# Kernel tuning notes

Hardware: AMD Instinct MI355X
Metric: run time of the kernel (lower is better)

The kernel has to match this reference:

```python
import jax, jax.numpy as jnp
import numpy as np

NUM_CAPS_OUT = 10
NUM_NODES = 32 * 6 * 6  # 1152
IN_DIM = 8
OUT_DIM = 16
ROUTING_ITERS = 3


def squash(x):
    # scale = |x|^2/(1+|x|^2); out = scale * x/|x|  (no epsilon, faithful to torch)
    sn = jnp.sum(x * x, axis=-1, keepdims=True)
    return sn / (1.0 + sn) * x / jnp.sqrt(sn)


def setup_inputs() -> dict:
    key = jax.random.key(0)
    ks = jax.random.split(key, 6)
    B = 512
    images = jax.random.normal(ks[0], (B, 1, 28, 28), dtype=jnp.float32)
    # ConvLayer: Conv2d(1, 256, k=9, s=1) with bias
    conv1_w = jax.random.normal(ks[1], (256, 1, 9, 9), dtype=jnp.float32) * 0.05
    conv1_b = jnp.zeros((256,), dtype=jnp.float32)
    prim_w = jax.random.normal(ks[2], (8 * 32, 256, 9, 9), dtype=jnp.float32) * 0.01
    prim_b = jnp.zeros((8 * 32,), dtype=jnp.float32)
    # DigitCaps weight: torch.randn(10, 1152, 8, 16)
    W = jax.random.normal(ks[3], (NUM_CAPS_OUT, NUM_NODES, IN_DIM, OUT_DIM), dtype=jnp.float32)
    return {"images": images, "conv1_w": conv1_w, "conv1_b": conv1_b,
            "prim_w": prim_w, "prim_b": prim_b, "W": W}


def reference(images, conv1_w, conv1_b, prim_w, prim_b, W):
    B = images.shape[0]
    dn = ('NCHW', 'OIHW', 'NCHW')
    # ConvLayer: 28x28 -> 20x20, 256 channels, ReLU
    x = jax.lax.conv_general_dilated(images, conv1_w, (1, 1), 'VALID', dimension_numbers=dn)
    x = jax.nn.relu(x + conv1_b[None, :, None, None])  # [B,256,20,20]
    # PrimaryCaps: 8 stacked convs -> [B, 8*32, 6, 6]; each capsule viewed as (32*6*6,)
    u = jax.lax.conv_general_dilated(x, prim_w, (2, 2), 'VALID', dimension_numbers=dn)
    u = u + prim_b[None, :, None, None]
    u = u.reshape(B, 8, NUM_NODES).transpose(0, 2, 1)  # [B,1152,8]
    u = squash(u)
    # DigitCaps: u_hat[c,b,n,o] = sum_i u[b,n,i] * W[c,n,i,o]
    u_hat = jnp.einsum('bni,cnio->cbno', u, W)  # [10,B,1152,16]
    # Dynamic routing (3 iterations). b_ij kept as [...,1]: torch replicates it
    # across the 16 out dims identically, so math is unchanged.
    b_ij = jnp.zeros(u_hat.shape[:-1] + (1,), dtype=u_hat.dtype)
    v_j = None
    for it in range(ROUTING_ITERS):
        c_ij = jax.nn.softmax(b_ij, axis=2)            # softmax over nodes
        s_j = jnp.sum(c_ij * u_hat, axis=2, keepdims=True)  # [10,B,1,16]
        v_j = squash(s_j)
        if it < ROUTING_ITERS - 1:
            a_ij = jnp.sum(u_hat * v_j, axis=-1, keepdims=True)  # [10,B,1152,1]
            b_ij = b_ij + a_ij
    # squeeze -> [10,B,16], transpose(0,1) -> [B,10,16]
    return v_j[:, :, 0, :].transpose(1, 0, 2)
```

## Files before the change

### kernel.cpp

```cpp
#include <hip/hip_runtime.h>
#include <hip/hip_bf16.h>
#include <cstddef>
#include <cstdint>

typedef __attribute__((ext_vector_type(8))) short v8s;
typedef __attribute__((ext_vector_type(16))) float v16f;

#define GLDS(SRC, DST) __builtin_amdgcn_global_load_lds( \
    (const __attribute__((address_space(1))) void*)(SRC), \
    (__attribute__((address_space(3))) void*)(DST), 16, 0, 0)

__device__ __forceinline__ void bf16split(float x, unsigned short& h, unsigned short& l) {
    union { float f; unsigned u; } a; a.f = x;
    unsigned r = a.u + 0x7fff + ((a.u >> 16) & 1);
    h = (unsigned short)(r >> 16);
    union { unsigned u; float f; } hb; hb.u = (unsigned)h << 16;
    union { float f; unsigned u; } b; b.f = x - hb.f;
    unsigned r2 = b.u + 0x7fff + ((b.u >> 16) & 1);
    l = (unsigned short)(r2 >> 16);
}

__global__ __launch_bounds__(256) void prep_kernel(
    const float* __restrict__ cw, const float* __restrict__ pw,
    float* __restrict__ wT1, char* __restrict__ wpk)
{
    int idx = blockIdx.x * 256 + threadIdx.x;
    if (idx < 81 * 256) {
        int k = idx >> 8, oc = idx & 255;
        wT1[idx] = cw[oc * 81 + k];
    }
    int Q = idx & 2047;
    int slab = idx >> 11;
    int D = Q << 4;
    int R = D >> 9;
    int v = (D & 511) ^ ((R & 31) << 4);
    int h = v >> 7, pl = (v >> 6) & 1, icb = v & 63;
    int ch = h * 64 + R;
    int g = slab / 81, k = slab - g * 81;
    int ic0 = g * 32 + (icb >> 1);
    const float* src = pw + ((size_t)ch * 256 + ic0) * 81 + k;
    v8s ov;
#pragma unroll
    for (int j = 0; j < 8; ++j) {
        unsigned short hh, ll; bf16split(src[(size_t)j * 81], hh, ll);
        ov[j] = (short)(pl ? ll : hh);
    }
    *(v8s*)(wpk + (size_t)slab * 32768 + D) = ov;
}

__global__ __launch_bounds__(256) void conv1_kernel(
    const float* __restrict__ img,
    const float* __restrict__ wT1,
    const float* __restrict__ bias,
    char* __restrict__ xc2,
    int b0)
{
    const int bl = blockIdx.x;
    const int oc = threadIdx.x;
    __shared__ __align__(16) float im[784];
    const float* ib = img + (size_t)(b0 + bl) * 784;
    for (int e = oc; e < 784; e += 256) im[e] = ib[e];
    float w[81];
#pragma unroll
    for (int k = 0; k < 81; ++k) w[k] = wT1[k * 256 + oc];
    float bv = bias[oc];
    __syncthreads();
    char* ob = xc2 + (size_t)bl * 409600;
    for (int oy = 0; oy < 20; ++oy) {
        float a[20];
#pragma unroll
        for (int ox = 0; ox < 20; ++ox) a[ox] = bv;
        for (int ky = 0; ky < 9; ++ky) {
            const float* rp = &im[(oy + ky) * 28];
            float r[28];
#pragma unroll
            for (int q = 0; q < 7; ++q) {
                float4 v4 = *(const float4*)(rp + q * 4);
                r[q * 4] = v4.x; r[q * 4 + 1] = v4.y;
                r[q * 4 + 2] = v4.z; r[q * 4 + 3] = v4.w;
            }
#pragma unroll
            for (int kx = 0; kx < 9; ++kx) {
                float wv = w[ky * 9 + kx];
#pragma unroll
                for (int ox = 0; ox < 20; ++ox)
                    a[ox] = fmaf(wv, r[ox + kx], a[ox]);
            }
        }
#pragma unroll
        for (int ox = 0; ox < 20; ++ox) {
            float av = fmaxf(a[ox], 0.f);
            unsigned short h, l; bf16split(av, h, l);
            char* rp2 = ob + (size_t)(oy * 20 + ox) * 1024;
            *(unsigned short*)(rp2 + oc * 2) = h;
            *(unsigned short*)(rp2 + 512 + oc * 2) = l;
        }
    }
}

__global__ __launch_bounds__(512, 2) void gemm_kernel(
    const char* __restrict__ xc2,
    const char* __restrict__ wpk,
    float* __restrict__ part,
    int M)
{
    __shared__ __align__(128) char As[2][32768];
    __shared__ __align__(128) char Bs[2][32768];
    const int tid = threadIdx.x;
    const int w = tid >> 6, lane = tid & 63;
    const int wm = w & 3, wn = w >> 2;
    const int col = lane & 31, kg = lane >> 5;
    const int id = blockIdx.x;
    const int g = id & 7;
    const int m0 = (id >> 3) * 256;

    int pbase[4], asrc[4];
#pragma unroll
    for (int i = 0; i < 4; ++i) {
        int d = (w * 4 + i) * 1024 + lane * 16;
        int R = d >> 9;
        int v = (d & 511) ^ ((R & 31) << 4);
        int h = v >> 7, pl = (v >> 6) & 1, icb = v & 63;
        int m = m0 + 64 * h + R; if (m >= M) m = M - 1;
        int b = m / 36, s6 = m - b * 36;
        pbase[i] = b * 400 + (s6 / 6) * 40 + (s6 % 6) * 2;
        asrc[i] = pl * 512 + g * 64 + icb;
    }
    const char* wg = wpk + (size_t)g * 81 * 32768;

    v16f acc[2][4];
#pragma unroll
    for (int i = 0; i < 2; ++i)
#pragma unroll
        for (int j = 0; j < 4; ++j)
#pragma unroll
            for (int e = 0; e < 16; ++e) acc[i][j][e] = 0.f;

    auto stage = [&](int nb, int kk) {
        const int koff = (kk / 9) * 20 + (kk % 9);
#pragma unroll
        for (int i = 0; i < 4; ++i)
            GLDS(xc2 + (size_t)(pbase[i] + koff) * 1024 + asrc[i],
                 &As[nb][(w * 4 + i) * 1024]);
        const char* bs = wg + (size_t)kk * 32768;
#pragma unroll
        for (int i = 0; i < 4; ++i)
            GLDS(bs + (w * 4 + i) * 1024 + lane * 16,
                 &Bs[nb][(w * 4 + i) * 1024]);
    };

    stage(0, 0);
    __syncthreads();

    const int xr = col << 4;
    for (int k = 0; k < 81; ++k) {
        const int cur = k & 1;
        if (k < 80) stage(cur ^ 1, k + 1);
        const char* Ab = &As[cur][0];
        const char* Bb = &Bs[cur][0];
#pragma unroll
        for (int s = 0; s < 2; ++s) {
            const int vb = s * 32 + kg * 16;
            v8s Ah[2], Al[2], Bh[4], Bl[4];
#pragma unroll
            for (int fm = 0; fm < 2; ++fm) {
                const char* ap = Ab + (fm * 32 + col) * 512;
                Ah[fm] = *(const v8s*)(ap + ((wm * 128 + vb) ^ xr));
                Al[fm] = *(const v8s*)(ap + ((wm * 128 + 64 + vb) ^ xr));
            }
#pragma unroll
            for (int fn = 0; fn < 4; ++fn) {
                const char* bp = Bb + ((fn & 1) * 32 + col) * 512;
                const int ho = (wn * 2 + (fn >> 1)) * 128;
                Bh[fn] = *(const v8s*)(bp + ((ho + vb) ^ xr));
                Bl[fn] = *(const v8s*)(bp + ((ho + 64 + vb) ^ xr));
            }
            __builtin_amdgcn_s_setprio(1);
#pragma unroll
            for (int fn = 0; fn < 4; ++fn)
#pragma unroll
                for (int fm = 0; fm < 2; ++fm) {
                    acc[fm][fn] = __builtin_amdgcn_mfma_f32_32x32x16_bf16(Al[fm], Bh[fn], acc[fm][fn], 0, 0, 0);
                    acc[fm][fn] = __builtin_amdgcn_mfma_f32_32x32x16_bf16(Ah[fm], Bl[fn], acc[fm][fn], 0, 0, 0);
                    acc[fm][fn] = __builtin_amdgcn_mfma_f32_32x32x16_bf16(Ah[fm], Bh[fn], acc[fm][fn], 0, 0, 0);
                }
            __builtin_amdgcn_s_setprio(0);
        }
        if (k < 80) __syncthreads();
    }

    float* pg = part + (size_t)g * M * 256;
#pragma unroll
    for (int fm = 0; fm < 2; ++fm)
#pragma unroll
        for (int fn = 0; fn < 4; ++fn) {
            int ch = wn * 128 + fn * 32 + col;
#pragma unroll
            for (int rg = 0; rg < 16; ++rg) {
                int row = (rg & 3) + 8 * (rg >> 2) + 4 * kg;
                int m = m0 + wm * 64 + fm * 32 + row;
                if (m < M) pg[(size_t)m * 256 + ch] = acc[fm][fn][rg];
            }
        }
}

__global__ __launch_bounds__(256) void prim2u_kernel(
    const float* __restrict__ part, const float* __restrict__ pb,
    float* __restrict__ u, int M, int b0)
{
    __shared__ float p[64 * 257];
    __shared__ float bsh[256];
    const int tid = threadIdx.x;
    const int rows0 = blockIdx.x * 64;
    bsh[tid] = pb[tid];
#pragma unroll
    for (int j = 0; j < 16; ++j) {
        int e4 = j * 256 + tid;
        int row = e4 >> 6, c4 = (e4 & 63) << 2;
        int rr = rows0 + row; if (rr >= M) rr = M - 1;
        float4 a = make_float4(0.f, 0.f, 0.f, 0.f);
#pragma unroll
        for (int g = 0; g < 8; ++g) {
            float4 v = *(const float4*)(part + ((size_t)g * M + rr) * 256 + c4);
            a.x += v.x; a.y += v.y; a.z += v.z; a.w += v.w;
        }
        float* pp = &p[row * 257 + c4];
        pp[0] = a.x; pp[1] = a.y; pp[2] = a.z; pp[3] = a.w;
    }
    __syncthreads();
#pragma unroll
    for (int j = 0; j < 8; ++j) {
        int idx = j * 256 + tid;
        int row = idx & 63, cc = idx >> 6;
        int m = rows0 + row;
        if (m >= M) continue;
        int b = m / 36, s = m - b * 36;
        float p8[8]; float sn = 0.f;
#pragma unroll
        for (int d = 0; d < 8; ++d) {
            float v = p[row * 257 + d * 32 + cc] + bsh[d * 32 + cc];
            p8[d] = v; sn += v * v;
        }
        float fac = sqrtf(sn) / (1.0f + sn);
        float4 o0, o1;
        o0.x = fac * p8[0]; o0.y = fac * p8[1]; o0.z = fac * p8[2]; o0.w = fac * p8[3];
        o1.x = fac * p8[4]; o1.y = fac * p8[5]; o1.z = fac * p8[6]; o1.w = fac * p8[7];
        float* up = u + ((size_t)(b0 + b) * 1152 + cc * 36 + s) * 8;
        *(float4*)up = o0;
        *(float4*)(up + 4) = o1;
    }
}

__global__ __launch_bounds__(512) void routing_kernel(
    const float* __restrict__ u,
    const float* __restrict__ W,
    float* __restrict__ out,
    int B)
{
    const int b0 = blockIdx.x * 2;
    const int c = blockIdx.y;
    const int tid = threadIdx.x;
    __shared__ float uht[2][16][1152];
    __shared__ float bijs[2][1152];
    __shared__ float red[2][4 * 17];
    __shared__ float sred[2][17];
    __shared__ float mred[2][4];

    const float* __restrict__ Wc = W + (size_t)c * (1152 * 128);
    const int b1 = (b0 + 1 < B) ? b0 + 1 : b0;
    const float* __restrict__ ub0 = u + (size_t)b0 * 9216;
    const float* __restrict__ ub1 = u + (size_t)b1 * 9216;

    for (int n = tid; n < 1152; n += 512) {
        const float4* p0 = (const float4*)(ub0 + n * 8);
        const float4* p1 = (const float4*)(ub1 + n * 8);
        float4 a0 = p0[0], a1 = p0[1], c0 = p1[0], c1 = p1[1];
        float uu0[8] = {a0.x, a0.y, a0.z, a0.w, a1.x, a1.y, a1.z, a1.w};
        float uu1[8] = {c0.x, c0.y, c0.z, c0.w, c1.x, c1.y, c1.z, c1.w};
        float acc0[16], acc1[16];
#pragma unroll
        for (int o = 0; o < 16; ++o) { acc0[o] = 0.f; acc1[o] = 0.f; }
        const float* wn = Wc + n * 128;
#pragma unroll
        for (int i = 0; i < 8; ++i)
#pragma unroll
            for (int o = 0; o < 16; ++o) {
                float wv = wn[i * 16 + o];
                acc0[o] = fmaf(uu0[i], wv, acc0[o]);
                acc1[o] = fmaf(uu1[i], wv, acc1[o]);
            }
#pragma unroll
        for (int o = 0; o < 16; ++o) { uht[0][o][n] = acc0[o]; uht[1][o][n] = acc1[o]; }
        bijs[0][n] = 0.f; bijs[1][n] = 0.f;
    }
    __syncthreads();

    const int img = tid >> 8, t = tid & 255;
    const int wid = t >> 6, lane = t & 63;
    const float* __restrict__ UHT = &uht[img][0][0];
    float* __restrict__ bij = bijs[img];
    float* __restrict__ redi = red[img];
    float* __restrict__ sredi = sred[img];
    float* __restrict__ mredi = mred[img];

    float fac = 0.f, inv = 0.f;
    for (int it = 0; it < 3; ++it) {
        float m = -3.4e38f;
        for (int n = t; n < 1152; n += 256) m = fmaxf(m, bij[n]);
#pragma unroll
        for (int off = 32; off > 0; off >>= 1) m = fmaxf(m, __shfl_down(m, off));
        if (lane == 0) mredi[wid] = m;
        __syncthreads();
        float M = fmaxf(fmaxf(mredi[0], mredi[1]), fmaxf(mredi[2], mredi[3]));
        float se = 0.f;
        float sp[16];
#pragma unroll
        for (int o = 0; o < 16; ++o) sp[o] = 0.f;
        for (int n = t; n < 1152; n += 256) {
            float e = expf(bij[n] - M);
            se += e;
#pragma unroll
            for (int o = 0; o < 16; ++o) sp[o] = fmaf(e, UHT[o * 1152 + n], sp[o]);
        }
#pragma unroll
        for (int o = 0; o < 16; ++o)
#pragma unroll
            for (int off = 32; off > 0; off >>= 1) sp[o] += __shfl_down(sp[o], off);
#pragma unroll
        for (int off = 32; off > 0; off >>= 1) se += __shfl_down(se, off);
        if (lane == 0) {
#pragma unroll
            for (int o = 0; o < 16; ++o) redi[wid * 17 + o] = sp[o];
            redi[wid * 17 + 16] = se;
        }
        __syncthreads();
        if (t < 17)
            sredi[t] = redi[t] + redi[17 + t] + redi[34 + t] + redi[51 + t];
        __syncthreads();
        inv = 1.0f / sredi[16];
        float sn = 0.f;
        float sj[16];
#pragma unroll
        for (int o = 0; o < 16; ++o) { sj[o] = sredi[o] * inv; sn = fmaf(sj[o], sj[o], sn); }
        fac = sqrtf(sn) / (1.0f + sn);
        if (it < 2) {
            float v[16];
#pragma unroll
            for (int o = 0; o < 16; ++o) v[o] = fac * sj[o];
            for (int n = t; n < 1152; n += 256) {
                float a = 0.f;
#pragma unroll
                for (int o = 0; o < 16; ++o) a = fmaf(UHT[o * 1152 + n], v[o], a);
                bij[n] += a;
            }
        }
        __syncthreads();
    }
    if (t < 16 && b0 + img < B)
        out[((size_t)(b0 + img) * 10 + c) * 16 + t] = fac * (sredi[t] * inv);
}

extern "C" void kernel_launch(void* const* d_in, const int* in_sizes, int n_in,
                              void* d_out, int out_size, void* d_ws, size_t ws_size,
                              hipStream_t stream) {
    const float* images  = (const float*)d_in[0];
    const float* conv1_w = (const float*)d_in[1];
    const float* conv1_b = (const float*)d_in[2];
    const float* prim_w  = (const float*)d_in[3];
    const float* prim_b  = (const float*)d_in[4];
    const float* W       = (const float*)d_in[5];
    float* out = (float*)d_out;

    const int B = in_sizes[0] / 784;

    char* wsb = (char*)d_ws;
    float* u = (float*)wsb;
    size_t off = (size_t)B * 1152 * 8 * 4;
    float* wT1 = (float*)(wsb + off);
    off += 81 * 256 * 4;
    off = (off + 1023) & ~(size_t)1023;
    char* wpk = wsb + off;
    off += (size_t)648 * 32768;
    size_t rem = (ws_size > off) ? ws_size - off : 0;
    const size_t perimg = 409600 + 294912;
    int Bc = (int)(rem / perimg);
    if (Bc > B) Bc = B;
    if (Bc >= 32) Bc &= ~31;
    if (Bc < 1) Bc = 1;

    prep_kernel<<<5184, 256, 0, stream>>>(conv1_w, prim_w, wT1, wpk);

    for (int b0 = 0; b0 < B; b0 += Bc) {
        int bc = (B - b0 < Bc) ? (B - b0) : Bc;
        char* xc2 = wsb + off;
        float* part = (float*)(xc2 + (size_t)Bc * 409600);
        conv1_kernel<<<bc, 256, 0, stream>>>(images, wT1, conv1_b, xc2, b0);
        int M = bc * 36;
        int Mtiles = (M + 255) / 256;
        gemm_kernel<<<Mtiles * 8, 512, 0, stream>>>(xc2, wpk, part, M);
        prim2u_kernel<<<(M + 63) / 64, 256, 0, stream>>>(part, prim_b, u, M, b0);
    }
    dim3 rg((B + 1) / 2, 10);
    routing_kernel<<<rg, 512, 0, stream>>>(u, W, out, B);
}
```

Measured before the change: 1.196 ms.

## Retile primary-caps GEMM to 192-row tiles and restructure prep and routing kernels

The GEMM moves from a 256x256 block tile to 192 rows by 256 channels, with a 2x4 warp layout (each warp does 3x2 MFMA fragments) and launch bounds relaxed to one block per CU. On M=18432 this gives 96 M-tiles instead of 72, so the 8-group grid holds more blocks and spreads better across CUs. The weight-prep kernel now stages one output channel's weights in LDS so global reads are coalesced. The routing kernel uses a flattened 1D grid and float4 weight loads. The GEMM change trades less reuse of each staged B tile, and possibly lower occupancy, for better load balance.

```diff
diff --git a/kernel.cpp b/kernel.cpp
--- a/kernel.cpp
+++ b/kernel.cpp
@@ -24,28 +24,29 @@
     const float* __restrict__ cw, const float* __restrict__ pw,
     float* __restrict__ wT1, char* __restrict__ wpk)
 {
-    int idx = blockIdx.x * 256 + threadIdx.x;
-    if (idx < 81 * 256) {
-        int k = idx >> 8, oc = idx & 255;
-        wT1[idx] = cw[oc * 81 + k];
-    }
-    int Q = idx & 2047;
-    int slab = idx >> 11;
-    int D = Q << 4;
-    int R = D >> 9;
-    int v = (D & 511) ^ ((R & 31) << 4);
-    int h = v >> 7, pl = (v >> 6) & 1, icb = v & 63;
-    int ch = h * 64 + R;
-    int g = slab / 81, k = slab - g * 81;
-    int ic0 = g * 32 + (icb >> 1);
-    const float* src = pw + ((size_t)ch * 256 + ic0) * 81 + k;
-    v8s ov;
-#pragma unroll
-    for (int j = 0; j < 8; ++j) {
-        unsigned short hh, ll; bf16split(src[(size_t)j * 81], hh, ll);
-        ov[j] = (short)(pl ? ll : hh);
-    }
-    *(v8s*)(wpk + (size_t)slab * 32768 + D) = ov;
+    __shared__ float lf[20736];
+    const int tid = threadIdx.x;
+    const int ch = blockIdx.x;
+    const float* ps = pw + (size_t)ch * 20736;
+    for (int e = tid; e < 20736; e += 256) lf[e] = ps[e];
+    if (tid < 81) wT1[tid * 256 + ch] = cw[ch * 81 + tid];
+    __syncthreads();
+    const int R = ch & 63, h = ch >> 6;
+    const int xr = (R & 31) << 4;
+    for (int idx = tid; idx < 5184; idx += 256) {
+        int q = idx & 3, pl = (idx >> 2) & 1, sk = idx >> 3;
+        int g = sk / 81, k = sk - g * 81;
+        int icb0 = q * 16;
+        int ic0 = g * 32 + (icb0 >> 1);
+        v8s ov;
+#pragma unroll
+        for (int j = 0; j < 8; ++j) {
+            unsigned short hh, ll; bf16split(lf[(ic0 + j) * 81 + k], hh, ll);
+            ov[j] = (short)(pl ? ll : hh);
+        }
+        int D = R * 512 + ((h * 128 + pl * 64 + icb0) ^ xr);
+        *(v8s*)(wpk + (size_t)sk * 32768 + D) = ov;
+    }
 }
 
 __global__ __launch_bounds__(256) void conv1_kernel(
@@ -98,50 +99,59 @@
     }
 }
 
-__global__ __launch_bounds__(512, 2) void gemm_kernel(
+__global__ __launch_bounds__(512, 1) void gemm_kernel(
     const char* __restrict__ xc2,
     const char* __restrict__ wpk,
     float* __restrict__ part,
     int M)
 {
-    __shared__ __align__(128) char As[2][32768];
+    __shared__ __align__(128) char As[2][24576];
     __shared__ __align__(128) char Bs[2][32768];
     const int tid = threadIdx.x;
     const int w = tid >> 6, lane = tid & 63;
-    const int wm = w & 3, wn = w >> 2;
+    const int wm = w & 1, wn = w >> 1;
     const int col = lane & 31, kg = lane >> 5;
     const int id = blockIdx.x;
     const int g = id & 7;
-    const int m0 = (id >> 3) * 256;
-
-    int pbase[4], asrc[4];
-#pragma unroll
-    for (int i = 0; i < 4; ++i) {
-        int d = (w * 4 + i) * 1024 + lane * 16;
+    const int m0 = (id >> 3) * 192;
+
+    int pbase[3], asrc[3];
+#pragma unroll
+    for (int i = 0; i < 3; ++i) {
+        int d = (w * 3 + i) * 1024 + lane * 16;
         int R = d >> 9;
         int v = (d & 511) ^ ((R & 31) << 4);
         int h = v >> 7, pl = (v >> 6) & 1, icb = v & 63;
-        int m = m0 + 64 * h + R; if (m >= M) m = M - 1;
+        int m = m0 + 48 * h + R; if (m >= M) m = M - 1;
         int b = m / 36, s6 = m - b * 36;
         pbase[i] = b * 400 + (s6 / 6) * 40 + (s6 % 6) * 2;
         asrc[i] = pl * 512 + g * 64 + icb;
     }
+    int Abase[3], Ahof[3], Axor[3];
+#pragma unroll
+    for (int fm = 0; fm < 3; ++fm) {
+        int m = wm * 96 + fm * 32 + col;
+        int h = m / 48, R = m - h * 48;
+        Abase[fm] = R * 512;
+        Ahof[fm] = h * 128;
+        Axor[fm] = (R & 31) << 4;
+    }
     const char* wg = wpk + (size_t)g * 81 * 32768;
 
-    v16f acc[2][4];
-#pragma unroll
-    for (int i = 0; i < 2; ++i)
-#pragma unroll
-        for (int j = 0; j < 4; ++j)
+    v16f acc[3][2];
+#pragma unroll
+    for (int i = 0; i < 3; ++i)
+#pragma unroll
+        for (int j = 0; j < 2; ++j)
 #pragma unroll
             for (int e = 0; e < 16; ++e) acc[i][j][e] = 0.f;
 
     auto stage = [&](int nb, int kk) {
         const int koff = (kk / 9) * 20 + (kk % 9);
 #pragma unroll
-        for (int i = 0; i < 4; ++i)
+        for (int i = 0; i < 3; ++i)
             GLDS(xc2 + (size_t)(pbase[i] + koff) * 1024 + asrc[i],
-                 &As[nb][(w * 4 + i) * 1024]);
+                 &As[nb][(w * 3 + i) * 1024]);
         const char* bs = wg + (size_t)kk * 32768;
 #pragma unroll
         for (int i = 0; i < 4; ++i)
@@ -161,25 +171,24 @@
 #pragma unroll
         for (int s = 0; s < 2; ++s) {
             const int vb = s * 32 + kg * 16;
-            v8s Ah[2], Al[2], Bh[4], Bl[4];
-#pragma unroll
-            for (int fm = 0; fm < 2; ++fm) {
-                const char* ap = Ab + (fm * 32 + col) * 512;
-                Ah[fm] = *(const v8s*)(ap + ((wm * 128 + vb) ^ xr));
-                Al[fm] = *(const v8s*)(ap + ((wm * 128 + 64 + vb) ^ xr));
-            }
-#pragma unroll
-            for (int fn = 0; fn < 4; ++fn) {
-                const char* bp = Bb + ((fn & 1) * 32 + col) * 512;
-                const int ho = (wn * 2 + (fn >> 1)) * 128;
-                Bh[fn] = *(const v8s*)(bp + ((ho + vb) ^ xr));
-                Bl[fn] = *(const v8s*)(bp + ((ho + 64 + vb) ^ xr));
+            v8s Ah[3], Al[3], Bh[2], Bl[2];
+#pragma unroll
+            for (int fm = 0; fm < 3; ++fm) {
+                const char* ap = Ab + Abase[fm];
+                Ah[fm] = *(const v8s*)(ap + ((Ahof[fm] + vb) ^ Axor[fm]));
+                Al[fm] = *(const v8s*)(ap + ((Ahof[fm] + 64 + vb) ^ Axor[fm]));
+            }
+#pragma unroll
+            for (int fn = 0; fn < 2; ++fn) {
+                const char* bp = Bb + (fn * 32 + col) * 512;
+                Bh[fn] = *(const v8s*)(bp + ((wn * 128 + vb) ^ xr));
+                Bl[fn] = *(const v8s*)(bp + ((wn * 128 + 64 + vb) ^ xr));
             }
             __builtin_amdgcn_s_setprio(1);
 #pragma unroll
-            for (int fn = 0; fn < 4; ++fn)
-#pragma unroll
-                for (int fm = 0; fm < 2; ++fm) {
+            for (int fn = 0; fn < 2; ++fn)
+#pragma unroll
+                for (int fm = 0; fm < 3; ++fm) {
                     acc[fm][fn] = __builtin_amdgcn_mfma_f32_32x32x16_bf16(Al[fm], Bh[fn], acc[fm][fn], 0, 0, 0);
                     acc[fm][fn] = __builtin_amdgcn_mfma_f32_32x32x16_bf16(Ah[fm], Bl[fn], acc[fm][fn], 0, 0, 0);
                     acc[fm][fn] = __builtin_amdgcn_mfma_f32_32x32x16_bf16(Ah[fm], Bh[fn], acc[fm][fn], 0, 0, 0);
@@ -191,14 +200,14 @@
 
     float* pg = part + (size_t)g * M * 256;
 #pragma unroll
-    for (int fm = 0; fm < 2; ++fm)
-#pragma unroll
-        for (int fn = 0; fn < 4; ++fn) {
-            int ch = wn * 128 + fn * 32 + col;
+    for (int fm = 0; fm < 3; ++fm)
+#pragma unroll
+        for (int fn = 0; fn < 2; ++fn) {
+            int ch = wn * 64 + fn * 32 + col;
 #pragma unroll
             for (int rg = 0; rg < 16; ++rg) {
                 int row = (rg & 3) + 8 * (rg >> 2) + 4 * kg;
-                int m = m0 + wm * 64 + fm * 32 + row;
+                int m = m0 + wm * 96 + fm * 32 + row;
                 if (m < M) pg[(size_t)m * 256 + ch] = acc[fm][fn][rg];
             }
         }
@@ -255,10 +264,12 @@
     const float* __restrict__ u,
     const float* __restrict__ W,
     float* __restrict__ out,
-    int B)
+    int B, int npairs)
 {
-    const int b0 = blockIdx.x * 2;
-    const int c = blockIdx.y;
+    const int id = blockIdx.x;
+    const int c = id / npairs;
+    const int pair = id - c * npairs;
+    const int b0 = pair * 2;
     const int tid = threadIdx.x;
     __shared__ float uht[2][16][1152];
     __shared__ float bijs[2][1152];
@@ -280,14 +291,20 @@
         float acc0[16], acc1[16];
 #pragma unroll
         for (int o = 0; o < 16; ++o) { acc0[o] = 0.f; acc1[o] = 0.f; }
-        const float* wn = Wc + n * 128;
+        const float4* w4 = (const float4*)(Wc + n * 128);
 #pragma unroll
         for (int i = 0; i < 8; ++i)
 #pragma unroll
-            for (int o = 0; o < 16; ++o) {
-                float wv = wn[i * 16 + o];
-                acc0[o] = fmaf(uu0[i], wv, acc0[o]);
-                acc1[o] = fmaf(uu1[i], wv, acc1[o]);
+            for (int q = 0; q < 4; ++q) {
+                float4 wv = w4[i * 4 + q];
+                acc0[q * 4 + 0] = fmaf(uu0[i], wv.x, acc0[q * 4 + 0]);
+                acc0[q * 4 + 1] = fmaf(uu0[i], wv.y, acc0[q * 4 + 1]);
+                acc0[q * 4 + 2] = fmaf(uu0[i], wv.z, acc0[q * 4 + 2]);
+                acc0[q * 4 + 3] = fmaf(uu0[i], wv.w, acc0[q * 4 + 3]);
+                acc1[q * 4 + 0] = fmaf(uu1[i], wv.x, acc1[q * 4 + 0]);
+                acc1[q * 4 + 1] = fmaf(uu1[i], wv.y, acc1[q * 4 + 1]);
+                acc1[q * 4 + 2] = fmaf(uu1[i], wv.z, acc1[q * 4 + 2]);
+                acc1[q * 4 + 3] = fmaf(uu1[i], wv.w, acc1[q * 4 + 3]);
             }
 #pragma unroll
         for (int o = 0; o < 16; ++o) { uht[0][o][n] = acc0[o]; uht[1][o][n] = acc1[o]; }
@@ -388,7 +405,7 @@
     if (Bc >= 32) Bc &= ~31;
     if (Bc < 1) Bc = 1;
 
-    prep_kernel<<<5184, 256, 0, stream>>>(conv1_w, prim_w, wT1, wpk);
+    prep_kernel<<<256, 256, 0, stream>>>(conv1_w, prim_w, wT1, wpk);
 
     for (int b0 = 0; b0 < B; b0 += Bc) {
         int bc = (B - b0 < Bc) ? (B - b0) : Bc;
@@ -396,10 +413,10 @@
         float* part = (float*)(xc2 + (size_t)Bc * 409600);
         conv1_kernel<<<bc, 256, 0, stream>>>(images, wT1, conv1_b, xc2, b0);
         int M = bc * 36;
-        int Mtiles = (M + 255) / 256;
+        int Mtiles = (M + 191) / 192;
         gemm_kernel<<<Mtiles * 8, 512, 0, stream>>>(xc2, wpk, part, M);
         prim2u_kernel<<<(M + 63) / 64, 256, 0, stream>>>(part, prim_b, u, M, b0);
     }
-    dim3 rg((B + 1) / 2, 10);
-    routing_kernel<<<rg, 512, 0, stream>>>(u, W, out, B);
-}
+    int npairs = (B + 1) / 2;
+    routing_kernel<<<npairs * 10, 512, 0, stream>>>(u, W, out, B, npairs);
+}
```

Result: no change. 1.199 ms (+0.2%).
